# Performance work log

Hardware: AMD Instinct MI355X
Metric: run time of the kernel (lower is better)

The kernel has to match this reference:

```python
import jax, jax.numpy as jnp
import numpy as np

B, E, IN = 2048, 256, 2          # batch_size, n_evals, in_features
C, D1, D2, O = 100, 20, 20, 100  # n_centers, dim1, dim2, out_dims
H1, H2, Z = 128, 64, 20          # VAE hidden1, hidden2, z_dim


def _lin(key, fan_in, fan_out):
    s = 1.0 / np.sqrt(fan_in)
    return jax.random.uniform(key, (fan_in, fan_out), minval=-s, maxval=s)


def setup_inputs() -> dict:
    key = jax.random.key(0)
    ks = jax.random.split(key, 20)
    inp = {
        'x': jax.random.normal(ks[0], (B, E, IN), dtype=jnp.float32),
        'eps': jax.random.normal(ks[1], (B, Z), dtype=jnp.float32),
        'alpha': jnp.asarray(1.0, dtype=jnp.float32),
        'centers': jax.random.normal(ks[2], (C, IN), dtype=jnp.float32),
        # PHI MLP
        'W1': _lin(ks[3], C, D1), 'b1': jnp.zeros((D1,)),
        'W2': _lin(ks[4], D1, D2), 'b2': jnp.zeros((D2,)),
        'W3': _lin(ks[5], D2, O), 'b3': jnp.zeros((O,)),
        # per-sample beta Linear(out_dims, 1): weight (B,O), bias (B,)
        'beta_W': jax.random.normal(ks[6], (B, O), dtype=jnp.float32) * (1.0 / np.sqrt(O)),
        'beta_b': jnp.zeros((B,)),
        # VAE encoder
        'eW1': _lin(ks[7], O, H1), 'eb1': jnp.zeros((H1,)),
        'eW2': _lin(ks[8], H1, H2), 'eb2': jnp.zeros((H2,)),
        'Wmu': _lin(ks[9], H2, Z), 'bmu': jnp.zeros((Z,)),
        'Wlv': _lin(ks[10], H2, Z), 'blv': jnp.zeros((Z,)),
        # VAE decoder
        'dW1': _lin(ks[11], Z, H2), 'db1': jnp.zeros((H2,)),
        'dW2': _lin(ks[12], H2, H1), 'db2': jnp.zeros((H1,)),
        'dW3': _lin(ks[13], H1, O), 'db3': jnp.zeros((O,)),
    }
    return inp


def reference(x, eps, alpha, centers, W1, b1, W2, b2, W3, b3, beta_W, beta_b,
              eW1, eb1, eW2, eb2, Wmu, bmu, Wlv, blv, dW1, db1, dW2, db2, dW3, db3):
    # --- PHI: RBF features over trainable centers, then tanh MLP ---
    # squared distances: (B,E,C)
    d2 = jnp.sum((x[:, :, None, :] - centers[None, None, :, :]) ** 2, axis=-1)
    feat = jnp.exp(-alpha * d2)
    h = jnp.tanh(feat @ W1 + b1)
    h = jnp.tanh(h @ W2 + b2)
    phi_x = h @ W3 + b3                                   # (B,E,O)

    # --- y1: per-sample Linear(out_dims,1), batched as one einsum ---
    y1 = jnp.einsum('beo,bo->be', phi_x, beta_W) + beta_b[:, None]

    # --- VAE over stacked beta weights (B,O) ---
    he = jax.nn.relu(beta_W @ eW1 + eb1)
    he = jax.nn.relu(he @ eW2 + eb2)
    mu = he @ Wmu + bmu
    logvar = he @ Wlv + blv
    z = mu + jnp.exp(0.5 * logvar) * eps
    hd = jax.nn.relu(z @ dW1 + db1)
    hd = jax.nn.relu(hd @ dW2 + db2)
    recon = hd @ dW3 + db3                                # (B,O)

    # --- y2: phi_x[i] @ recon[i] + bias_i, batched ---
    y2 = jnp.einsum('beo,bo->be', phi_x, recon) + beta_b[:, None]
    return (y1, y2, mu, logvar)
```

## Files before the change

### kernel.cpp

```cpp
#include <hip/hip_runtime.h>

#define Bn 2048
#define En 256
#define INn 2
#define Cn 100
#define D1n 20
#define D2n 20
#define On 100
#define H1n 128
#define H2n 64
#define Zn 20


__device__ __forceinline__ float tanh_fast(float t) {
    float at = fabsf(t);
    float e  = exp2f(-2.885390082f * at);
    float r  = (1.0f - e) * __builtin_amdgcn_rcpf(1.0f + e);
    return t < 0.0f ? -r : r;
}

__global__ __launch_bounds__(256) void pivae_fused(
    const float* __restrict__ x,      const float* __restrict__ eps,
    const float* __restrict__ alpha_p,const float* __restrict__ centers,
    const float* __restrict__ W1,     const float* __restrict__ b1,
    const float* __restrict__ W2,     const float* __restrict__ b2,
    const float* __restrict__ W3,     const float* __restrict__ b3,
    const float* __restrict__ beta_W, const float* __restrict__ beta_b,
    const float* __restrict__ eW1,    const float* __restrict__ eb1,
    const float* __restrict__ eW2,    const float* __restrict__ eb2,
    const float* __restrict__ Wmu,    const float* __restrict__ bmu,
    const float* __restrict__ Wlv,    const float* __restrict__ blv,
    const float* __restrict__ dW1,    const float* __restrict__ db1,
    const float* __restrict__ dW2,    const float* __restrict__ db2,
    const float* __restrict__ dW3,    const float* __restrict__ db3,
    float* __restrict__ out_y1, float* __restrict__ out_y2,
    float* __restrict__ out_mu, float* __restrict__ out_lv)
{
    const int b = blockIdx.x;
    const int t = threadIdx.x;

    __shared__ __align__(16) float c0l[Cn];
    __shared__ __align__(16) float c1l[Cn];
    __shared__ __align__(16) float w1l[Cn * D1n];
    __shared__ __align__(16) float w2l[D1n * D2n];
    __shared__ __align__(16) float w3l[D2n * On];
    __shared__ __align__(16) float b1l[D1n];
    __shared__ __align__(16) float b2l[D2n];
    __shared__ __align__(16) float b3l[On];
    __shared__ __align__(16) float bwl[On];
    __shared__ __align__(16) float rcl[On];
    __shared__ float he1[H1n];
    __shared__ float he2[H2n];
    __shared__ float zz[Zn];
    __shared__ float hd1[H2n];
    __shared__ float hd2[H1n];

    if (t < Cn) {
        const float2 cv = *reinterpret_cast<const float2*>(centers + 2 * t);
        c0l[t] = cv.x;
        c1l[t] = cv.y;
        bwl[t] = beta_W[b * On + t];
        b3l[t] = b3[t];
    }
    for (int i = t; i < Cn * D1n; i += 256) w1l[i] = W1[i];
    for (int i = t; i < D2n * On;  i += 256) w3l[i] = W3[i];
    for (int i = t; i < D1n * D2n; i += 256) w2l[i] = W2[i];
    if (t < D1n) b1l[t] = b1[t];
    if (t >= 64 && t < 64 + D2n) b2l[t - 64] = b2[t - 64];
    __syncthreads();

    if (t < H1n) {
        float a = eb1[t];
        #pragma unroll 4
        for (int i = 0; i < Cn; ++i) a += bwl[i] * eW1[i * H1n + t];
        he1[t] = fmaxf(a, 0.0f);
    }
    __syncthreads();
    if (t < H2n) {
        float a = eb2[t];
        #pragma unroll 4
        for (int i = 0; i < H1n; ++i) a += he1[i] * eW2[i * H2n + t];
        he2[t] = fmaxf(a, 0.0f);
    }
    __syncthreads();
    if (t < Zn) {
        float m = bmu[t], l = blv[t];
        #pragma unroll 4
        for (int i = 0; i < H2n; ++i) {
            float h = he2[i];
            m += h * Wmu[i * Zn + t];
            l += h * Wlv[i * Zn + t];
        }
        out_mu[b * Zn + t] = m;
        out_lv[b * Zn + t] = l;
        zz[t] = m + exp2f(0.72134752f * l) * eps[b * Zn + t];
    }
    __syncthreads();
    if (t < H2n) {
        float a = db1[t];
        #pragma unroll
        for (int i = 0; i < Zn; ++i) a += zz[i] * dW1[i * H2n + t];
        hd1[t] = fmaxf(a, 0.0f);
    }
    __syncthreads();
    if (t < H1n) {
        float a = db2[t];
        #pragma unroll 4
        for (int i = 0; i < H2n; ++i) a += hd1[i] * dW2[i * H1n + t];
        hd2[t] = fmaxf(a, 0.0f);
    }
    __syncthreads();
    if (t < On) {
        float a = db3[t];
        #pragma unroll 4
        for (int i = 0; i < H1n; ++i) a += hd2[i] * dW3[i * On + t];
        rcl[t] = a;
    }
    __syncthreads();

    const float2 xv = *reinterpret_cast<const float2*>(x + ((size_t)b * En + t) * 2);
    const float na  = -alpha_p[0] * 1.44269504f;

    float h[D1n];
    #pragma unroll
    for (int j = 0; j < D1n; ++j) h[j] = 0.0f;
    for (int c = 0; c < Cn; ++c) {
        const float dx0 = xv.x - c0l[c];
        const float dx1 = xv.y - c1l[c];
        const float f = exp2f(na * (dx0 * dx0 + dx1 * dx1));
        const float4* wr = reinterpret_cast<const float4*>(&w1l[c * D1n]);
        #pragma unroll
        for (int q = 0; q < 5; ++q) {
            const float4 v = wr[q];
            h[4 * q + 0] = fmaf(f, v.x, h[4 * q + 0]);
            h[4 * q + 1] = fmaf(f, v.y, h[4 * q + 1]);
            h[4 * q + 2] = fmaf(f, v.z, h[4 * q + 2]);
            h[4 * q + 3] = fmaf(f, v.w, h[4 * q + 3]);
        }
    }
    #pragma unroll
    for (int j = 0; j < D1n; ++j) h[j] = tanh_fast(h[j] + b1l[j]);

    float g[D2n];
    #pragma unroll
    for (int j = 0; j < D2n; ++j) g[j] = b2l[j];
    #pragma unroll
    for (int k = 0; k < D1n; ++k) {
        const float hk = h[k];
        const float4* wr = reinterpret_cast<const float4*>(&w2l[k * D2n]);
        #pragma unroll
        for (int q = 0; q < 5; ++q) {
            const float4 v = wr[q];
            g[4 * q + 0] = fmaf(hk, v.x, g[4 * q + 0]);
            g[4 * q + 1] = fmaf(hk, v.y, g[4 * q + 1]);
            g[4 * q + 2] = fmaf(hk, v.z, g[4 * q + 2]);
            g[4 * q + 3] = fmaf(hk, v.w, g[4 * q + 3]);
        }
    }
    #pragma unroll
    for (int j = 0; j < D2n; ++j) g[j] = tanh_fast(g[j]);

    const float bb = beta_b[b];
    float y1 = bb, y2 = bb;
    for (int o4 = 0; o4 < On / 4; ++o4) {
        float4 p = *reinterpret_cast<const float4*>(&b3l[o4 * 4]);
        #pragma unroll
        for (int k = 0; k < D2n; ++k) {
            const float gk = g[k];
            const float4 wv = *reinterpret_cast<const float4*>(&w3l[k * On + o4 * 4]);
            p.x = fmaf(gk, wv.x, p.x);
            p.y = fmaf(gk, wv.y, p.y);
            p.z = fmaf(gk, wv.z, p.z);
            p.w = fmaf(gk, wv.w, p.w);
        }
        const float4 bw = *reinterpret_cast<const float4*>(&bwl[o4 * 4]);
        const float4 rc = *reinterpret_cast<const float4*>(&rcl[o4 * 4]);
        y1 += p.x * bw.x + p.y * bw.y + p.z * bw.z + p.w * bw.w;
        y2 += p.x * rc.x + p.y * rc.y + p.z * rc.z + p.w * rc.w;
    }

    const size_t oidx = (size_t)b * En + t;
    out_y1[oidx] = y1;
    out_y2[oidx] = y2;
}

extern "C" void kernel_launch(void* const* d_in, const int* in_sizes, int n_in,
                              void* d_out, int out_size, void* d_ws, size_t ws_size,
                              hipStream_t stream)
{
    const float* x       = (const float*)d_in[0];
    const float* eps     = (const float*)d_in[1];
    const float* alpha   = (const float*)d_in[2];
    const float* centers = (const float*)d_in[3];
    const float* W1      = (const float*)d_in[4];
    const float* b1      = (const float*)d_in[5];
    const float* W2      = (const float*)d_in[6];
    const float* b2      = (const float*)d_in[7];
    const float* W3      = (const float*)d_in[8];
    const float* b3      = (const float*)d_in[9];
    const float* beta_W  = (const float*)d_in[10];
    const float* beta_b  = (const float*)d_in[11];
    const float* eW1     = (const float*)d_in[12];
    const float* eb1     = (const float*)d_in[13];
    const float* eW2     = (const float*)d_in[14];
    const float* eb2     = (const float*)d_in[15];
    const float* Wmu     = (const float*)d_in[16];
    const float* bmu     = (const float*)d_in[17];
    const float* Wlv     = (const float*)d_in[18];
    const float* blv     = (const float*)d_in[19];
    const float* dW1     = (const float*)d_in[20];
    const float* db1     = (const float*)d_in[21];
    const float* dW2     = (const float*)d_in[22];
    const float* db2     = (const float*)d_in[23];
    const float* dW3     = (const float*)d_in[24];
    const float* db3     = (const float*)d_in[25];

    float* out    = (float*)d_out;
    float* out_y1 = out;
    float* out_y2 = out + (size_t)Bn * En;
    float* out_mu = out + (size_t)2 * Bn * En;
    float* out_lv = out_mu + (size_t)Bn * Zn;

    pivae_fused<<<dim3(Bn), dim3(256), 0, stream>>>(
        x, eps, alpha, centers, W1, b1, W2, b2, W3, b3, beta_W, beta_b,
        eW1, eb1, eW2, eb2, Wmu, bmu, Wlv, blv,
        dW1, db1, dW2, db2, dW3, db3,
        out_y1, out_y2, out_mu, out_lv);
}
```

Measured before the change: 229.7 us.

## Fold W3 into per-sample vectors, expand RBF distance, process two samples per block

Precomputes u = W3·beta_W and W3·recon per sample (plus bias scalars), so the per-eval 20x100 output layer and two 100-long dot products collapse into two 20-long dot products. Expands the squared distance into x·c and norm terms folded into precomputed center constants, which removes a few ops per center. Each block now handles two samples, and each thread handles two evals, which halves block count and amortizes weight staging and the VAE's serial phases. The cost is more registers per thread (two 20-wide accumulator sets) and a slightly different floating-point summation order.

Result: faster. 200.9 us (-12.5%).

```diff
diff --git a/kernel.cpp b/kernel.cpp
--- a/kernel.cpp
+++ b/kernel.cpp
@@ -19,7 +19,7 @@
     return t < 0.0f ? -r : r;
 }
 
-__global__ __launch_bounds__(256) void pivae_fused(
+__global__ __launch_bounds__(256) void pivae_fused2(
     const float* __restrict__ x,      const float* __restrict__ eps,
     const float* __restrict__ alpha_p,const float* __restrict__ centers,
     const float* __restrict__ W1,     const float* __restrict__ b1,
@@ -36,152 +36,176 @@
     float* __restrict__ out_y1, float* __restrict__ out_y2,
     float* __restrict__ out_mu, float* __restrict__ out_lv)
 {
-    const int b = blockIdx.x;
-    const int t = threadIdx.x;
-
-    __shared__ __align__(16) float c0l[Cn];
-    __shared__ __align__(16) float c1l[Cn];
-    __shared__ __align__(16) float w1l[Cn * D1n];
-    __shared__ __align__(16) float w2l[D1n * D2n];
-    __shared__ __align__(16) float w3l[D2n * On];
-    __shared__ __align__(16) float b1l[D1n];
-    __shared__ __align__(16) float b2l[D2n];
-    __shared__ __align__(16) float b3l[On];
-    __shared__ __align__(16) float bwl[On];
-    __shared__ __align__(16) float rcl[On];
-    __shared__ float he1[H1n];
-    __shared__ float he2[H2n];
-    __shared__ float zz[Zn];
-    __shared__ float hd1[H2n];
-    __shared__ float hd2[H1n];
+    const int t  = threadIdx.x;
+    const int b0 = blockIdx.x * 2;
+
+    __shared__ __align__(16) float  w1l[Cn * D1n];
+    __shared__ __align__(16) float  w2l[D1n * D2n];
+    __shared__ __align__(16) float4 ctr[Cn];
+    __shared__ __align__(16) float  b1l[D1n];
+    __shared__ __align__(16) float  b2l[D2n];
+    __shared__ __align__(16) float  bwl[2][On];
+    __shared__ __align__(16) float  rcl[2][On];
+    __shared__ float he1[2][H1n];
+    __shared__ float he2[2][H2n];
+    __shared__ float zzs[2][Zn];
+    __shared__ float hd1[2][H2n];
+    __shared__ float hd2[2][H1n];
+    __shared__ float u1l[2][Zn];
+    __shared__ float u2l[2][Zn];
+    __shared__ float s12[2][2];
+
+    const float na = -alpha_p[0] * 1.44269504f;
 
     if (t < Cn) {
         const float2 cv = *reinterpret_cast<const float2*>(centers + 2 * t);
-        c0l[t] = cv.x;
-        c1l[t] = cv.y;
-        bwl[t] = beta_W[b * On + t];
-        b3l[t] = b3[t];
+        ctr[t] = make_float4(-2.0f * na * cv.x, -2.0f * na * cv.y,
+                             na * (cv.x * cv.x + cv.y * cv.y), 0.0f);
     }
     for (int i = t; i < Cn * D1n; i += 256) w1l[i] = W1[i];
-    for (int i = t; i < D2n * On;  i += 256) w3l[i] = W3[i];
     for (int i = t; i < D1n * D2n; i += 256) w2l[i] = W2[i];
     if (t < D1n) b1l[t] = b1[t];
-    if (t >= 64 && t < 64 + D2n) b2l[t - 64] = b2[t - 64];
-    __syncthreads();
-
-    if (t < H1n) {
-        float a = eb1[t];
-        #pragma unroll 4
-        for (int i = 0; i < Cn; ++i) a += bwl[i] * eW1[i * H1n + t];
-        he1[t] = fmaxf(a, 0.0f);
-    }
-    __syncthreads();
-    if (t < H2n) {
-        float a = eb2[t];
-        #pragma unroll 4
-        for (int i = 0; i < H1n; ++i) a += he1[i] * eW2[i * H2n + t];
-        he2[t] = fmaxf(a, 0.0f);
-    }
-    __syncthreads();
-    if (t < Zn) {
-        float m = bmu[t], l = blv[t];
-        #pragma unroll 4
-        for (int i = 0; i < H2n; ++i) {
-            float h = he2[i];
-            m += h * Wmu[i * Zn + t];
-            l += h * Wlv[i * Zn + t];
+    if (t >= 32 && t < 32 + D2n) b2l[t - 32] = b2[t - 32];
+    if (t < 2 * On) { int s = t / On, o = t - s * On; bwl[s][o] = beta_W[(b0 + s) * On + o]; }
+    __syncthreads();
+
+    {
+        const int s = t >> 7, j = t & 127;
+        float a = eb1[j];
+        #pragma unroll 4
+        for (int i = 0; i < Cn; ++i) a += bwl[s][i] * eW1[i * H1n + j];
+        he1[s][j] = fmaxf(a, 0.0f);
+    }
+    __syncthreads();
+    if (t < 128) {
+        const int s = t >> 6, j = t & 63;
+        float a = eb2[j];
+        #pragma unroll 4
+        for (int i = 0; i < H1n; ++i) a += he1[s][i] * eW2[i * H2n + j];
+        he2[s][j] = fmaxf(a, 0.0f);
+    }
+    __syncthreads();
+    if (t < 64) {
+        const int s = t >> 5, j = t & 31;
+        if (j < Zn) {
+            float m = bmu[j], l = blv[j];
+            #pragma unroll 4
+            for (int i = 0; i < H2n; ++i) {
+                const float h = he2[s][i];
+                m += h * Wmu[i * Zn + j];
+                l += h * Wlv[i * Zn + j];
+            }
+            out_mu[(b0 + s) * Zn + j] = m;
+            out_lv[(b0 + s) * Zn + j] = l;
+            zzs[s][j] = m + exp2f(0.72134752f * l) * eps[(b0 + s) * Zn + j];
         }
-        out_mu[b * Zn + t] = m;
-        out_lv[b * Zn + t] = l;
-        zz[t] = m + exp2f(0.72134752f * l) * eps[b * Zn + t];
-    }
-    __syncthreads();
-    if (t < H2n) {
-        float a = db1[t];
+    }
+    __syncthreads();
+    if (t < 128) {
+        const int s = t >> 6, j = t & 63;
+        float a = db1[j];
         #pragma unroll
-        for (int i = 0; i < Zn; ++i) a += zz[i] * dW1[i * H2n + t];
-        hd1[t] = fmaxf(a, 0.0f);
-    }
-    __syncthreads();
-    if (t < H1n) {
-        float a = db2[t];
-        #pragma unroll 4
-        for (int i = 0; i < H2n; ++i) a += hd1[i] * dW2[i * H1n + t];
-        hd2[t] = fmaxf(a, 0.0f);
-    }
-    __syncthreads();
-    if (t < On) {
-        float a = db3[t];
-        #pragma unroll 4
-        for (int i = 0; i < H1n; ++i) a += hd2[i] * dW3[i * On + t];
-        rcl[t] = a;
-    }
-    __syncthreads();
-
-    const float2 xv = *reinterpret_cast<const float2*>(x + ((size_t)b * En + t) * 2);
-    const float na  = -alpha_p[0] * 1.44269504f;
-
-    float h[D1n];
-    #pragma unroll
-    for (int j = 0; j < D1n; ++j) h[j] = 0.0f;
+        for (int i = 0; i < Zn; ++i) a += zzs[s][i] * dW1[i * H2n + j];
+        hd1[s][j] = fmaxf(a, 0.0f);
+    }
+    __syncthreads();
+    {
+        const int s = t >> 7, j = t & 127;
+        float a = db2[j];
+        #pragma unroll 4
+        for (int i = 0; i < H2n; ++i) a += hd1[s][i] * dW2[i * H1n + j];
+        hd2[s][j] = fmaxf(a, 0.0f);
+    }
+    __syncthreads();
+    if (t < 2 * On) {
+        const int s = t / On, o = t - s * On;
+        float a = db3[o];
+        #pragma unroll 4
+        for (int i = 0; i < H1n; ++i) a += hd2[s][i] * dW3[i * On + o];
+        rcl[s][o] = a;
+    }
+    __syncthreads();
+    if (t < 80) {
+        const int s = t / 40, r = t - 40 * s, which = r / 20, k = r - 20 * which;
+        const float* src = which ? rcl[s] : bwl[s];
+        float a = 0.0f;
+        #pragma unroll 4
+        for (int o = 0; o < On; ++o) a += W3[k * On + o] * src[o];
+        float (*dst)[Zn] = which ? u2l : u1l;
+        dst[s][k] = a;
+    } else if (t < 84) {
+        const int idx = t - 80, s = idx >> 1, which = idx & 1;
+        const float* src = which ? rcl[s] : bwl[s];
+        float a = beta_b[b0 + s];
+        #pragma unroll 4
+        for (int o = 0; o < On; ++o) a += b3[o] * src[o];
+        s12[s][which] = a;
+    }
+    __syncthreads();
+
+    const int s  = t >> 7;
+    const int e0 = (t & 127) * 2;
+    const float4 xv = *reinterpret_cast<const float4*>(x + ((size_t)(b0 + s) * En + e0) * INn);
+    const float A0 = na * (xv.x * xv.x + xv.y * xv.y);
+    const float A1 = na * (xv.z * xv.z + xv.w * xv.w);
+
+    float h0[D1n], h1[D1n];
+    #pragma unroll
+    for (int j = 0; j < D1n; ++j) { h0[j] = 0.0f; h1[j] = 0.0f; }
+
     for (int c = 0; c < Cn; ++c) {
-        const float dx0 = xv.x - c0l[c];
-        const float dx1 = xv.y - c1l[c];
-        const float f = exp2f(na * (dx0 * dx0 + dx1 * dx1));
+        const float4 cc = ctr[c];
+        const float arg0 = fmaf(xv.x, cc.x, fmaf(xv.y, cc.y, A0 + cc.z));
+        const float arg1 = fmaf(xv.z, cc.x, fmaf(xv.w, cc.y, A1 + cc.z));
+        const float f0 = exp2f(arg0);
+        const float f1 = exp2f(arg1);
         const float4* wr = reinterpret_cast<const float4*>(&w1l[c * D1n]);
         #pragma unroll
         for (int q = 0; q < 5; ++q) {
             const float4 v = wr[q];
-            h[4 * q + 0] = fmaf(f, v.x, h[4 * q + 0]);
-            h[4 * q + 1] = fmaf(f, v.y, h[4 * q + 1]);
-            h[4 * q + 2] = fmaf(f, v.z, h[4 * q + 2]);
-            h[4 * q + 3] = fmaf(f, v.w, h[4 * q + 3]);
+            h0[4*q+0] = fmaf(f0, v.x, h0[4*q+0]);  h1[4*q+0] = fmaf(f1, v.x, h1[4*q+0]);
+            h0[4*q+1] = fmaf(f0, v.y, h0[4*q+1]);  h1[4*q+1] = fmaf(f1, v.y, h1[4*q+1]);
+            h0[4*q+2] = fmaf(f0, v.z, h0[4*q+2]);  h1[4*q+2] = fmaf(f1, v.z, h1[4*q+2]);
+            h0[4*q+3] = fmaf(f0, v.w, h0[4*q+3]);  h1[4*q+3] = fmaf(f1, v.w, h1[4*q+3]);
         }
     }
     #pragma unroll
-    for (int j = 0; j < D1n; ++j) h[j] = tanh_fast(h[j] + b1l[j]);
-
-    float g[D2n];
-    #pragma unroll
-    for (int j = 0; j < D2n; ++j) g[j] = b2l[j];
+    for (int j = 0; j < D1n; ++j) {
+        h0[j] = tanh_fast(h0[j] + b1l[j]);
+        h1[j] = tanh_fast(h1[j] + b1l[j]);
+    }
+
+    float g0[D2n], g1[D2n];
+    #pragma unroll
+    for (int j = 0; j < D2n; ++j) { g0[j] = b2l[j]; g1[j] = b2l[j]; }
     #pragma unroll
     for (int k = 0; k < D1n; ++k) {
-        const float hk = h[k];
+        const float hk0 = h0[k], hk1 = h1[k];
         const float4* wr = reinterpret_cast<const float4*>(&w2l[k * D2n]);
         #pragma unroll
         for (int q = 0; q < 5; ++q) {
             const float4 v = wr[q];
-            g[4 * q + 0] = fmaf(hk, v.x, g[4 * q + 0]);
-            g[4 * q + 1] = fmaf(hk, v.y, g[4 * q + 1]);
-            g[4 * q + 2] = fmaf(hk, v.z, g[4 * q + 2]);
-            g[4 * q + 3] = fmaf(hk, v.w, g[4 * q + 3]);
+            g0[4*q+0] = fmaf(hk0, v.x, g0[4*q+0]);  g1[4*q+0] = fmaf(hk1, v.x, g1[4*q+0]);
+            g0[4*q+1] = fmaf(hk0, v.y, g0[4*q+1]);  g1[4*q+1] = fmaf(hk1, v.y, g1[4*q+1]);
+            g0[4*q+2] = fmaf(hk0, v.z, g0[4*q+2]);  g1[4*q+2] = fmaf(hk1, v.z, g1[4*q+2]);
+            g0[4*q+3] = fmaf(hk0, v.w, g0[4*q+3]);  g1[4*q+3] = fmaf(hk1, v.w, g1[4*q+3]);
         }
     }
-    #pragma unroll
-    for (int j = 0; j < D2n; ++j) g[j] = tanh_fast(g[j]);
-
-    const float bb = beta_b[b];
-    float y1 = bb, y2 = bb;
-    for (int o4 = 0; o4 < On / 4; ++o4) {
-        float4 p = *reinterpret_cast<const float4*>(&b3l[o4 * 4]);
-        #pragma unroll
-        for (int k = 0; k < D2n; ++k) {
-            const float gk = g[k];
-            const float4 wv = *reinterpret_cast<const float4*>(&w3l[k * On + o4 * 4]);
-            p.x = fmaf(gk, wv.x, p.x);
-            p.y = fmaf(gk, wv.y, p.y);
-            p.z = fmaf(gk, wv.z, p.z);
-            p.w = fmaf(gk, wv.w, p.w);
-        }
-        const float4 bw = *reinterpret_cast<const float4*>(&bwl[o4 * 4]);
-        const float4 rc = *reinterpret_cast<const float4*>(&rcl[o4 * 4]);
-        y1 += p.x * bw.x + p.y * bw.y + p.z * bw.z + p.w * bw.w;
-        y2 += p.x * rc.x + p.y * rc.y + p.z * rc.z + p.w * rc.w;
-    }
-
-    const size_t oidx = (size_t)b * En + t;
-    out_y1[oidx] = y1;
-    out_y2[oidx] = y2;
+
+    float y1_0 = s12[s][0], y1_1 = s12[s][0];
+    float y2_0 = s12[s][1], y2_1 = s12[s][1];
+    #pragma unroll
+    for (int k = 0; k < D2n; ++k) {
+        const float gk0 = tanh_fast(g0[k]);
+        const float gk1 = tanh_fast(g1[k]);
+        const float uk1 = u1l[s][k], uk2 = u2l[s][k];
+        y1_0 = fmaf(gk0, uk1, y1_0);  y1_1 = fmaf(gk1, uk1, y1_1);
+        y2_0 = fmaf(gk0, uk2, y2_0);  y2_1 = fmaf(gk1, uk2, y2_1);
+    }
+
+    const size_t oidx = (size_t)(b0 + s) * En + e0;
+    *reinterpret_cast<float2*>(out_y1 + oidx) = make_float2(y1_0, y1_1);
+    *reinterpret_cast<float2*>(out_y2 + oidx) = make_float2(y2_0, y2_1);
 }
 
 extern "C" void kernel_launch(void* const* d_in, const int* in_sizes, int n_in,
@@ -221,7 +245,7 @@
     float* out_mu = out + (size_t)2 * Bn * En;
     float* out_lv = out_mu + (size_t)Bn * Zn;
 
-    pivae_fused<<<dim3(Bn), dim3(256), 0, stream>>>(
+    pivae_fused2<<<dim3(Bn / 2), dim3(256), 0, stream>>>(
         x, eps, alpha, centers, W1, b1, W2, b2, W3, b3, beta_W, beta_b,
         eW1, eb1, eW2, eb2, Wmu, bmu, Wlv, blv,
         dW1, db1, dW2, db2, dW3, db3,
```
